# Kernel optimization log

Measured on AMD Instinct MI355X. Metric: run time of the kernel, lower is better.

## Reference

```python
import jax, jax.numpy as jnp
import numpy as np

B, T, N, D, NH = 4, 256, 8, 128, 4
SCALES = (1, 2, 3, 5)
LAGS = (1, 2, 3)
MLP_H = 32
NL_SCALE = 0.1
CMIN, CMAX = -2.5, 2.0
L_ENC = 2  # num_attn_layers


def _ln(x, g, b, eps=1e-5):
    m = x.mean(-1, keepdims=True)
    v = ((x - m) ** 2).mean(-1, keepdims=True)
    return (x - m) * jax.lax.rsqrt(v + eps) * g + b


def _gelu(x):
    return jax.nn.gelu(x, approximate=False)


def _mha(q, k, v, Wq, bq, Wk, bk, Wv, bv, Wo, bo, nh):
    Bq, Lq, Dm = q.shape
    Lk = k.shape[1]
    hd = Dm // nh
    qh = (q @ Wq.T + bq).reshape(Bq, Lq, nh, hd).transpose(0, 2, 1, 3)
    kh = (k @ Wk.T + bk).reshape(Bq, Lk, nh, hd).transpose(0, 2, 1, 3)
    vh = (v @ Wv.T + bv).reshape(Bq, Lk, nh, hd).transpose(0, 2, 1, 3)
    s = jnp.einsum('bhqd,bhkd->bhqk', qh, kh) / jnp.sqrt(jnp.float32(hd))
    p = jax.nn.softmax(s, axis=-1)
    o = jnp.einsum('bhqk,bhkd->bhqd', p, vh).transpose(0, 2, 1, 3).reshape(Bq, Lq, Dm)
    return o @ Wo.T + bo


def setup_inputs() -> dict:
    key = jax.random.key(0)
    ks = jax.random.split(key, 24)
    def w(k, shape, s=0.02):
        return s * jax.random.normal(k, shape, jnp.float32)
    inp = {}
    inp['visible_states'] = jax.random.uniform(ks[0], (B, T, N), jnp.float32) + 0.05
    inp['state_emb'] = jax.random.normal(ks[1], (B, T, N, D), jnp.float32)
    # LearnedBaseline params
    inp['r5'] = 0.1 * jnp.ones((N,), jnp.float32)
    A = 0.02 * jax.random.normal(ks[2], (N, N), jnp.float32)
    inp['A55'] = A.at[jnp.arange(N), jnp.arange(N)].set(-0.2)
    inp['bl_bias'] = jnp.zeros((N,), jnp.float32)
    inp['nl_W1'] = w(ks[3], (MLP_H, N), 0.1); inp['nl_b1'] = jnp.zeros((MLP_H,), jnp.float32)
    inp['nl_W2'] = w(ks[4], (N, MLP_H), 0.1); inp['nl_b2'] = jnp.zeros((N,), jnp.float32)
    # ResidualEncoder input MLP
    IN_DIM = len(SCALES) * (1 + len(LAGS))  # 16
    inp['mlp_W1'] = w(ks[5], (D, IN_DIM), 0.1); inp['mlp_b1'] = jnp.zeros((D,), jnp.float32)
    inp['mlp_W2'] = w(ks[6], (D, D)); inp['mlp_b2'] = jnp.zeros((D,), jnp.float32)
    inp['mlp_ln_g'] = jnp.ones((D,), jnp.float32); inp['mlp_ln_b'] = jnp.zeros((D,), jnp.float32)
    # ResidualEncoder transformer layers (stacked over L_ENC layers)
    inp['enc_qkv_W'] = w(ks[7], (L_ENC, 3 * D, D)); inp['enc_qkv_b'] = jnp.zeros((L_ENC, 3 * D), jnp.float32)
    inp['enc_out_W'] = w(ks[8], (L_ENC, D, D)); inp['enc_out_b'] = jnp.zeros((L_ENC, D), jnp.float32)
    inp['enc_ln1_g'] = jnp.ones((L_ENC, D), jnp.float32); inp['enc_ln1_b'] = jnp.zeros((L_ENC, D), jnp.float32)
    inp['enc_ff_W1'] = w(ks[9], (L_ENC, 2 * D, D)); inp['enc_ff_b1'] = jnp.zeros((L_ENC, 2 * D), jnp.float32)
    inp['enc_ff_W2'] = w(ks[10], (L_ENC, D, 2 * D)); inp['enc_ff_b2'] = jnp.zeros((L_ENC, D), jnp.float32)
    inp['enc_ln2_g'] = jnp.ones((L_ENC, D), jnp.float32); inp['enc_ln2_b'] = jnp.zeros((L_ENC, D), jnp.float32)
    # CrossAttentionFusion
    inp['ca_Wq'] = w(ks[11], (D, D)); inp['ca_bq'] = jnp.zeros((D,), jnp.float32)
    inp['ca_Wk'] = w(ks[12], (D, D)); inp['ca_bk'] = jnp.zeros((D,), jnp.float32)
    inp['ca_Wv'] = w(ks[13], (D, D)); inp['ca_bv'] = jnp.zeros((D,), jnp.float32)
    inp['ca_Wo'] = w(ks[14], (D, D)); inp['ca_bo'] = jnp.zeros((D,), jnp.float32)
    inp['ca_ln1_g'] = jnp.ones((D,), jnp.float32); inp['ca_ln1_b'] = jnp.zeros((D,), jnp.float32)
    inp['ca_ff_W1'] = w(ks[15], (4 * D, 2 * D)); inp['ca_ff_b1'] = jnp.zeros((4 * D,), jnp.float32)
    inp['ca_ff_W2'] = w(ks[16], (D, 4 * D)); inp['ca_ff_b2'] = jnp.zeros((D,), jnp.float32)
    inp['ca_ln2_g'] = jnp.ones((D,), jnp.float32); inp['ca_ln2_b'] = jnp.zeros((D,), jnp.float32)
    return inp


def _forward(visible_states, state_emb, r5, A55, bl_bias, nl_W1, nl_b1, nl_W2, nl_b2,
             mlp_W1, mlp_b1, mlp_W2, mlp_b2, mlp_ln_g, mlp_ln_b,
             enc_qkv_W, enc_qkv_b, enc_out_W, enc_out_b, enc_ln1_g, enc_ln1_b,
             enc_ff_W1, enc_ff_b1, enc_ff_W2, enc_ff_b2, enc_ln2_g, enc_ln2_b,
             ca_Wq, ca_bq, ca_Wk, ca_bk, ca_Wv, ca_bv, ca_Wo, ca_bo,
             ca_ln1_g, ca_ln1_b, ca_ff_W1, ca_ff_b1, ca_ff_W2, ca_ff_b2,
             ca_ln2_g, ca_ln2_b):
    # ---- LearnedBaseline on x_t = visible_states[:, :-1] ----
    safe = jnp.clip(visible_states, 1e-6, None)
    logx = jnp.log(safe)
    x_t = visible_states[:, :-1]  # (B,T-1,N)
    lin = r5 + jnp.einsum('btn,mn->btm', x_t, A55)
    nl = _gelu(x_t @ nl_W1.T + nl_b1) @ nl_W2.T + nl_b2
    b1 = lin + NL_SCALE * nl + bl_bias  # (B,T-1,N)
    # ---- MultiScaleResidual ----
    res_list = []
    for k in SCALES:
        actual = jnp.clip(logx[:, k:] - logx[:, :-k], CMIN * k, CMAX * k)  # (B,T-k,N)
        bk = b1[:, 0:T - k]
        for i in range(1, k):
            bk = bk + b1[:, i:i + T - k]
        res = actual - bk
        res_list.append(jnp.pad(res, ((0, 0), (0, k), (0, 0))))
    residuals = jnp.stack(res_list, axis=-1)  # (B,T,N,S)
    # ---- ResidualEncoder: takens delays ----
    feats = [residuals] + [jnp.pad(residuals, ((0, 0), (lag, 0), (0, 0), (0, 0)))[:, :T]
                           for lag in LAGS]
    x = jnp.concatenate(feats, axis=-1)  # (B,T,N,16)
    x = _gelu(x @ mlp_W1.T + mlp_b1)
    x = _gelu(x @ mlp_W2.T + mlp_b2)
    x = _ln(x, mlp_ln_g, mlp_ln_b)
    # sinusoidal PE over time
    pos = jnp.arange(T, dtype=jnp.float32)[:, None]
    div = jnp.exp(jnp.arange(0, D, 2, dtype=jnp.float32) * (-jnp.log(10000.0) / D))
    pe = jnp.stack([jnp.sin(pos * div), jnp.cos(pos * div)], axis=-1).reshape(T, D)
    x = x + pe[None, :, None, :]
    # temporal self-attention over (B*N, T, D)
    xt = x.transpose(0, 2, 1, 3).reshape(B * N, T, D)
    for i in range(L_ENC):
        Wq, Wk, Wv = jnp.split(enc_qkv_W[i], 3, axis=0)
        bq, bk_, bv = jnp.split(enc_qkv_b[i], 3)
        a = _mha(xt, xt, xt, Wq, bq, Wk, bk_, Wv, bv, enc_out_W[i], enc_out_b[i], NH)
        xt = _ln(xt + a, enc_ln1_g[i], enc_ln1_b[i])
        ff = _gelu(xt @ enc_ff_W1[i].T + enc_ff_b1[i]) @ enc_ff_W2[i].T + enc_ff_b2[i]
        xt = _ln(xt + ff, enc_ln2_g[i], enc_ln2_b[i])
    residual_emb = xt.reshape(B, N, T, D).transpose(0, 2, 1, 3)  # (B,T,N,D)
    # ---- CrossAttentionFusion ----
    s = state_emb.reshape(B, T * N, D)
    r = residual_emb.reshape(B, T * N, D)
    a = _mha(s, r, r, ca_Wq, ca_bq, ca_Wk, ca_bk, ca_Wv, ca_bv, ca_Wo, ca_bo, NH)
    s = _ln(s + a, ca_ln1_g, ca_ln1_b)
    fused = _gelu(jnp.concatenate([s, r], axis=-1) @ ca_ff_W1.T + ca_ff_b1) @ ca_ff_W2.T + ca_ff_b2
    out = _ln(s + fused, ca_ln2_g, ca_ln2_b)
    return out.reshape(B, T, N, D)


def reference(visible_states, state_emb, r5, A55, bl_bias, nl_W1, nl_b1, nl_W2, nl_b2,
              mlp_W1, mlp_b1, mlp_W2, mlp_b2, mlp_ln_g, mlp_ln_b,
              enc_qkv_W, enc_qkv_b, enc_out_W, enc_out_b, enc_ln1_g, enc_ln1_b,
              enc_ff_W1, enc_ff_b1, enc_ff_W2, enc_ff_b2, enc_ln2_g, enc_ln2_b,
              ca_Wq, ca_bq, ca_Wk, ca_bk, ca_Wv, ca_bv, ca_Wo, ca_bo,
              ca_ln1_g, ca_ln1_b, ca_ff_W1, ca_ff_b1, ca_ff_W2, ca_ff_b2,
              ca_ln2_g, ca_ln2_b):
    return _forward(visible_states, state_emb, r5, A55, bl_bias, nl_W1, nl_b1, nl_W2, nl_b2,
                    mlp_W1, mlp_b1, mlp_W2, mlp_b2, mlp_ln_g, mlp_ln_b,
                    enc_qkv_W, enc_qkv_b, enc_out_W, enc_out_b, enc_ln1_g, enc_ln1_b,
                    enc_ff_W1, enc_ff_b1, enc_ff_W2, enc_ff_b2, enc_ln2_g, enc_ln2_b,
                    ca_Wq, ca_bq, ca_Wk, ca_bk, ca_Wv, ca_bv, ca_Wo, ca_bo,
                    ca_ln1_g, ca_ln1_b, ca_ff_W1, ca_ff_b1, ca_ff_W2, ca_ff_b2,
                    ca_ln2_g, ca_ln2_b)
```

## Files before the change

### kernel.cpp

```cpp
#include <hip/hip_runtime.h>
#include <math.h>

#define B_ 4
#define T_ 256
#define N_ 8
#define D_ 128
#define NH_ 4
#define HD_ 32
#define LENC_ 2
#define MLPH_ 32
#define NL_SCALE_ 0.1f

typedef __bf16 bf16;
typedef __attribute__((ext_vector_type(2))) __bf16 bf16x2;
typedef __attribute__((ext_vector_type(4))) __bf16 bf16x4;
typedef __attribute__((ext_vector_type(8))) __bf16 bf16x8;
typedef __attribute__((ext_vector_type(4))) float f32x4;

__device__ __forceinline__ f32x4 pv_mfma16(bf16x4 a, bf16x4 b, f32x4 c) {
#if __has_builtin(__builtin_amdgcn_mfma_f32_16x16x16_bf16)
    return __builtin_amdgcn_mfma_f32_16x16x16_bf16(a, b, c, 0, 0, 0);
#else
    typedef __attribute__((ext_vector_type(4))) short s4;
    union U { bf16x4 h; s4 s; };
    U ua, ub; ua.h = a; ub.h = b;
    return __builtin_amdgcn_mfma_f32_16x16x16bf16_1k(ua.s, ub.s, c, 0, 0, 0);
#endif
}

__device__ __forceinline__ float gelu_f(float x) {
    return 0.5f * x * (1.0f + erff(x * 0.7071067811865476f));
}

__global__ void k_prep(const float* __restrict__ eqkvW, const float* __restrict__ eoutW,
                       const float* __restrict__ eff1, const float* __restrict__ eff2,
                       const float* __restrict__ wq, const float* __restrict__ wk,
                       const float* __restrict__ wv, const float* __restrict__ wo,
                       const float* __restrict__ cff1, const float* __restrict__ cff2,
                       const float* __restrict__ mlpW2, const float* __restrict__ semb,
                       const float* __restrict__ bk, const float* __restrict__ bv,
                       bf16* __restrict__ Wpk, bf16* __restrict__ sembh,
                       float* __restrict__ bpk) {
    int i = blockIdx.x * 256 + threadIdx.x;
    if (i < 540672) {
        const float* src; int off;
        if      (i < 98304)  { src = eqkvW; off = 0; }
        else if (i < 131072) { src = eoutW; off = 98304; }
        else if (i < 196608) { src = eff1;  off = 131072; }
        else if (i < 262144) { src = eff2;  off = 196608; }
        else if (i < 278528) { src = wq;    off = 262144; }
        else if (i < 294912) { src = wk;    off = 278528; }
        else if (i < 311296) { src = wv;    off = 294912; }
        else if (i < 327680) { src = wo;    off = 311296; }
        else if (i < 458752) { src = cff1;  off = 327680; }
        else if (i < 524288) { src = cff2;  off = 458752; }
        else                 { src = mlpW2; off = 524288; }
        Wpk[i] = (bf16)src[i - off];
    } else if (i < 540672 + 1048576) {
        int j = i - 540672;
        sembh[j] = (bf16)semb[j];
    } else if (i < 540672 + 1048576 + 256) {
        int t = i - 540672 - 1048576;
        bpk[t] = (t < 128) ? bk[t] : bv[t - 128];
    }
}

__global__ void k_b1(const float* __restrict__ vs, const float* __restrict__ r5,
                     const float* __restrict__ A55, const float* __restrict__ bl_bias,
                     const float* __restrict__ nlW1, const float* __restrict__ nlb1,
                     const float* __restrict__ nlW2, const float* __restrict__ nlb2,
                     float* __restrict__ b1w) {
    int idx = blockIdx.x * blockDim.x + threadIdx.x;
    if (idx >= B_ * (T_ - 1)) return;
    int b = idx / (T_ - 1), t = idx % (T_ - 1);
    float x[N_];
    for (int n = 0; n < N_; n++) x[n] = vs[(b * T_ + t) * N_ + n];
    float h[MLPH_];
    for (int j = 0; j < MLPH_; j++) {
        float a = nlb1[j];
        for (int n = 0; n < N_; n++) a += x[n] * nlW1[j * N_ + n];
        h[j] = gelu_f(a);
    }
    for (int m = 0; m < N_; m++) {
        float lin = r5[m];
        for (int n = 0; n < N_; n++) lin += x[n] * A55[m * N_ + n];
        float nl = nlb2[m];
        for (int j = 0; j < MLPH_; j++) nl += h[j] * nlW2[m * MLPH_ + j];
        b1w[idx * N_ + m] = lin + NL_SCALE_ * nl + bl_bias[m];
    }
}

__global__ void k_mlp1(const float* __restrict__ vs, const float* __restrict__ b1w,
                       const float* __restrict__ W1, const float* __restrict__ b1,
                       bf16* __restrict__ H1h) {
    int tok = blockIdx.x;
    int d = threadIdx.x;
    int b = tok >> 11, t = (tok >> 3) & 255, n = tok & 7;
    __shared__ float f[16];
    if (d < 16) {
        const int SC[4] = {1, 2, 3, 5};
        int lag = d >> 2, si = d & 3, k = SC[si];
        int tp = t - lag;
        float r = 0.0f;
        if (tp >= 0 && tp < T_ - k) {
            float lx0 = logf(fmaxf(vs[(b * T_ + tp) * N_ + n], 1e-6f));
            float lx1 = logf(fmaxf(vs[(b * T_ + tp + k) * N_ + n], 1e-6f));
            float a = lx1 - lx0;
            a = fminf(fmaxf(a, -2.5f * (float)k), 2.0f * (float)k);
            float bk = 0.0f;
            for (int i = 0; i < k; i++) bk += b1w[(b * (T_ - 1) + tp + i) * N_ + n];
            r = a - bk;
        }
        f[d] = r;
    }
    __syncthreads();
    float a = b1[d];
    const float* w = W1 + d * 16;
#pragma unroll
    for (int c = 0; c < 16; c++) a += f[c] * w[c];
    H1h[(size_t)tok * 128 + d] = (bf16)gelu_f(a);
}

__device__ __forceinline__ void gemm4_body(
    int bid, const bf16* __restrict__ A, const bf16* __restrict__ W,
    const float* __restrict__ bias, float* __restrict__ Cf,
    bf16* __restrict__ Ch, bf16* __restrict__ dq, bf16* __restrict__ dk,
    bf16* __restrict__ dvv, int N, int K, int act, int mode) {
    int lane = threadIdx.x & 63;
    int wv = threadIdx.x >> 6;
    int c = lane & 15, g = lane >> 4;
    int nN = N >> 6;
    int tn = bid % nN, tm = bid / nN;
    int row0 = tm * 64 + wv * 16;
    int cb = tn * 64;

    const bf16x8* Ap  = (const bf16x8*)(A + (size_t)(row0 + c) * K) + g;
    const bf16x8* Wp0 = (const bf16x8*)(W + (size_t)(cb + c) * K) + g;
    const bf16x8* Wp1 = (const bf16x8*)(W + (size_t)(cb + 16 + c) * K) + g;
    const bf16x8* Wp2 = (const bf16x8*)(W + (size_t)(cb + 32 + c) * K) + g;
    const bf16x8* Wp3 = (const bf16x8*)(W + (size_t)(cb + 48 + c) * K) + g;
    f32x4 a0 = {0, 0, 0, 0}, a1 = {0, 0, 0, 0};
    f32x4 a2 = {0, 0, 0, 0}, a3 = {0, 0, 0, 0};
    int nk = K >> 5;
    for (int k = 0; k < nk; k++) {
        bf16x8 av = Ap[k * 4];
        a0 = __builtin_amdgcn_mfma_f32_16x16x32_bf16(av, Wp0[k * 4], a0, 0, 0, 0);
        a1 = __builtin_amdgcn_mfma_f32_16x16x32_bf16(av, Wp1[k * 4], a1, 0, 0, 0);
        a2 = __builtin_amdgcn_mfma_f32_16x16x32_bf16(av, Wp2[k * 4], a2, 0, 0, 0);
        a3 = __builtin_amdgcn_mfma_f32_16x16x32_bf16(av, Wp3[k * 4], a3, 0, 0, 0);
    }
    int rowb = row0 + g * 4;
#pragma unroll
    for (int ct = 0; ct < 4; ct++) {
        f32x4 acc = (ct == 0) ? a0 : (ct == 1) ? a1 : (ct == 2) ? a2 : a3;
        int col = cb + ct * 16 + c;
        float bvv = bias[col];
#pragma unroll
        for (int i = 0; i < 4; i++) {
            float v = acc[i] + bvv;
            if (act) v = gelu_f(v);
            int row = rowb + i;
            if (mode == 0) {
                if (Cf) Cf[(size_t)row * N + col] = v;
                if (Ch) Ch[(size_t)row * N + col] = (bf16)v;
            } else if (mode == 1) {
                int s = row >> 8, t = row & 255;
                int h = (col >> 5) & 3, d = col & 31;
                int sh = s * 4 + h;
                if (col < 128)      dq[((size_t)sh * 256 + t) * 32 + d] = (bf16)v;
                else if (col < 256) dk[((size_t)sh * 256 + t) * 32 + d] = (bf16)v;
                else                dvv[((size_t)sh * 32 + d) * 256 + t] = (bf16)v;
            } else if (mode == 2) {
                int b = row >> 11, ll = row & 2047;
                int h = col >> 5, d = col & 31;
                dq[((size_t)(b * 4 + h) * 2048 + ll) * 32 + d] = (bf16)v;
            } else {
                int b = row >> 11, n = (row >> 8) & 7, t = row & 255;
                int ll = t * 8 + n;
                int h = (col >> 5) & 3, d = col & 31;
                if (col < 128) dk[((size_t)(b * 4 + h) * 2048 + ll) * 32 + d] = (bf16)v;
                else           dvv[((size_t)(b * 4 + h) * 32 + d) * 2048 + ll] = (bf16)v;
            }
        }
    }
}

__global__ __launch_bounds__(256) void k_gemm4(
    const bf16* __restrict__ A, const bf16* __restrict__ W,
    const float* __restrict__ bias, bf16* __restrict__ dq,
    bf16* __restrict__ dk, bf16* __restrict__ dvv, int N, int K, int mode) {
    gemm4_body(blockIdx.x, A, W, bias, nullptr, nullptr, dq, dk, dvv,
               N, K, 0, mode);
}

__global__ __launch_bounds__(256) void k_qkvc(
    const bf16* __restrict__ sembh, const bf16* __restrict__ Wq,
    const float* __restrict__ bq, const bf16* __restrict__ X0h,
    const bf16* __restrict__ Wkv, const float* __restrict__ bkv,
    bf16* __restrict__ Qh, bf16* __restrict__ Kh, bf16* __restrict__ Vth) {
    if (blockIdx.x < 256)
        gemm4_body(blockIdx.x, sembh, Wq, bq, nullptr, nullptr,
                   Qh, nullptr, nullptr, 128, 128, 0, 2);
    else
        gemm4_body(blockIdx.x - 256, X0h, Wkv, bkv, nullptr, nullptr,
                   nullptr, Kh, Vth, 256, 128, 0, 3);
}

__global__ __launch_bounds__(256) void k_gemm_ln(
    const bf16* __restrict__ A, const bf16* __restrict__ W,
    const float* __restrict__ bias, int K,
    const float* __restrict__ resf,
    const float* __restrict__ g, const float* __restrict__ be,
    float* __restrict__ outf, bf16* __restrict__ outh, int hs, int flags) {
    __shared__ float S[32][132];
    int tid = threadIdx.x;
    int w = tid >> 6, lane = tid & 63;
    int c = lane & 15, gq = lane >> 4;
    int r0 = blockIdx.x * 32 + (w >> 1) * 16;
    int cb = (w & 1) * 64;

    const bf16x8* Ap  = (const bf16x8*)(A + (size_t)(r0 + c) * K) + gq;
    const bf16x8* Wp0 = (const bf16x8*)(W + (size_t)(cb + c) * K) + gq;
    const bf16x8* Wp1 = (const bf16x8*)(W + (size_t)(cb + 16 + c) * K) + gq;
    const bf16x8* Wp2 = (const bf16x8*)(W + (size_t)(cb + 32 + c) * K) + gq;
    const bf16x8* Wp3 = (const bf16x8*)(W + (size_t)(cb + 48 + c) * K) + gq;
    f32x4 a0 = {0, 0, 0, 0}, a1 = {0, 0, 0, 0};
    f32x4 a2 = {0, 0, 0, 0}, a3 = {0, 0, 0, 0};
    int nk = K >> 5;
    for (int k = 0; k < nk; k++) {
        bf16x8 av = Ap[k * 4];
        a0 = __builtin_amdgcn_mfma_f32_16x16x32_bf16(av, Wp0[k * 4], a0, 0, 0, 0);
        a1 = __builtin_amdgcn_mfma_f32_16x16x32_bf16(av, Wp1[k * 4], a1, 0, 0, 0);
        a2 = __builtin_amdgcn_mfma_f32_16x16x32_bf16(av, Wp2[k * 4], a2, 0, 0, 0);
        a3 = __builtin_amdgcn_mfma_f32_16x16x32_bf16(av, Wp3[k * 4], a3, 0, 0, 0);
    }
    int lrow = (w >> 1) * 16 + gq * 4;
    float b0 = bias[cb + c], b1v = bias[cb + 16 + c];
    float b2v = bias[cb + 32 + c], b3v = bias[cb + 48 + c];
#pragma unroll
    for (int r = 0; r < 4; r++) {
        float v0 = a0[r] + b0, v1 = a1[r] + b1v;
        float v2 = a2[r] + b2v, v3 = a3[r] + b3v;
        if (flags & 1) {
            v0 = gelu_f(v0); v1 = gelu_f(v1); v2 = gelu_f(v2); v3 = gelu_f(v3);
        }
        S[lrow + r][cb + c] = v0;       S[lrow + r][cb + 16 + c] = v1;
        S[lrow + r][cb + 32 + c] = v2;  S[lrow + r][cb + 48 + c] = v3;
    }
    __syncthreads();

    int row = tid >> 3, cg = tid & 7;
    int grow = blockIdx.x * 32 + row;
    int b = grow >> 11, t = (grow >> 3) & 255, n = grow & 7;
    int orow = (flags & 4) ? ((b * 8 + n) * 256 + t) : grow;
    float v[16];
#pragma unroll
    for (int j = 0; j < 16; j++) v[j] = S[row][cg * 16 + j];
    if (resf) {
        const float4* rp = (const float4*)(resf + (size_t)grow * 128 + cg * 16);
#pragma unroll
        for (int j4 = 0; j4 < 4; j4++) {
            float4 rv = rp[j4];
            v[4 * j4 + 0] += rv.x; v[4 * j4 + 1] += rv.y;
            v[4 * j4 + 2] += rv.z; v[4 * j4 + 3] += rv.w;
        }
    }
    float s = 0.0f;
#pragma unroll
    for (int j = 0; j < 16; j++) s += v[j];
    s += __shfl_xor(s, 1); s += __shfl_xor(s, 2); s += __shfl_xor(s, 4);
    float mean = s * (1.0f / 128.0f);
    float vs = 0.0f;
#pragma unroll
    for (int j = 0; j < 16; j++) { float d = v[j] - mean; vs += d * d; }
    vs += __shfl_xor(vs, 1); vs += __shfl_xor(vs, 2); vs += __shfl_xor(vs, 4);
    float rstd = rsqrtf(vs * (1.0f / 128.0f) + 1e-5f);
    float y[16];
#pragma unroll
    for (int j = 0; j < 16; j++) {
        int col = cg * 16 + j;
        y[j] = (v[j] - mean) * rstd * g[col] + be[col];
    }
    if (flags & 2) {
#pragma unroll
        for (int jj = 0; jj < 8; jj++) {
            int j2 = cg * 8 + jj;
            float freq = expf((float)(2 * j2) * (-9.210340371976184f / 128.0f));
            float ang = (float)t * freq;
            y[2 * jj] += sinf(ang);
            y[2 * jj + 1] += cosf(ang);
        }
    }
    if (outf) {
        float4* op = (float4*)(outf + (size_t)orow * 128 + cg * 16);
#pragma unroll
        for (int j4 = 0; j4 < 4; j4++) {
            float4 o; o.x = y[4 * j4]; o.y = y[4 * j4 + 1];
            o.z = y[4 * j4 + 2]; o.w = y[4 * j4 + 3];
            op[j4] = o;
        }
    }
    if (outh) {
        bf16x8* op = (bf16x8*)(outh + (size_t)orow * hs + cg * 16);
#pragma unroll
        for (int j8 = 0; j8 < 2; j8++) {
            bf16x8 o;
#pragma unroll
            for (int e = 0; e < 8; e++) o[e] = (bf16)y[8 * j8 + e];
            op[j8] = o;
        }
    }
}

__global__ __launch_bounds__(256) void k_enc_tail(
    const bf16* __restrict__ ATTh, const bf16* __restrict__ Wo,
    const float* __restrict__ bo, const float* __restrict__ X0res,
    const float* __restrict__ g1, const float* __restrict__ be1,
    const bf16* __restrict__ W1, const float* __restrict__ bf1,
    const bf16* __restrict__ W2, const float* __restrict__ bf2,
    const float* __restrict__ g2, const float* __restrict__ be2,
    float* __restrict__ X0out, bf16* __restrict__ X0hout) {
    __shared__ float S[32][132];
    __shared__ float X1f[32][132];
    __shared__ bf16 X1h[32][136];
    __shared__ bf16 H[32][264];
    int tid = threadIdx.x;
    int w = tid >> 6, lane = tid & 63;
    int c = lane & 15, gq = lane >> 4;
    int r0l = (w >> 1) * 16;
    int cb = (w & 1) * 64;
    int blk = blockIdx.x;
    const f32x4 zero = {0, 0, 0, 0};

    {
        const bf16x8* Ap  = (const bf16x8*)(ATTh + (size_t)(blk * 32 + r0l + c) * 128) + gq;
        const bf16x8* Wp0 = (const bf16x8*)(Wo + (size_t)(cb + c) * 128) + gq;
        const bf16x8* Wp1 = (const bf16x8*)(Wo + (size_t)(cb + 16 + c) * 128) + gq;
        const bf16x8* Wp2 = (const bf16x8*)(Wo + (size_t)(cb + 32 + c) * 128) + gq;
        const bf16x8* Wp3 = (const bf16x8*)(Wo + (size_t)(cb + 48 + c) * 128) + gq;
        f32x4 a0 = zero, a1 = zero, a2 = zero, a3 = zero;
#pragma unroll
        for (int k = 0; k < 4; k++) {
            bf16x8 av = Ap[k * 4];
            a0 = __builtin_amdgcn_mfma_f32_16x16x32_bf16(av, Wp0[k * 4], a0, 0, 0, 0);
            a1 = __builtin_amdgcn_mfma_f32_16x16x32_bf16(av, Wp1[k * 4], a1, 0, 0, 0);
            a2 = __builtin_amdgcn_mfma_f32_16x16x32_bf16(av, Wp2[k * 4], a2, 0, 0, 0);
            a3 = __builtin_amdgcn_mfma_f32_16x16x32_bf16(av, Wp3[k * 4], a3, 0, 0, 0);
        }
        int lrow = r0l + gq * 4;
        float b0 = bo[cb + c], b1v = bo[cb + 16 + c];
        float b2v = bo[cb + 32 + c], b3v = bo[cb + 48 + c];
#pragma unroll
        for (int r = 0; r < 4; r++) {
            S[lrow + r][cb + c] = a0[r] + b0;
            S[lrow + r][cb + 16 + c] = a1[r] + b1v;
            S[lrow + r][cb + 32 + c] = a2[r] + b2v;
            S[lrow + r][cb + 48 + c] = a3[r] + b3v;
        }
    }
    __syncthreads();
    {
        int row = tid >> 3, cg = tid & 7;
        float v[16];
        const float4* rp = (const float4*)(X0res + (size_t)(blk * 32 + row) * 128 + cg * 16);
#pragma unroll
        for (int j4 = 0; j4 < 4; j4++) {
            float4 rv = rp[j4];
            v[4 * j4 + 0] = S[row][cg * 16 + 4 * j4 + 0] + rv.x;
            v[4 * j4 + 1] = S[row][cg * 16 + 4 * j4 + 1] + rv.y;
            v[4 * j4 + 2] = S[row][cg * 16 + 4 * j4 + 2] + rv.z;
            v[4 * j4 + 3] = S[row][cg * 16 + 4 * j4 + 3] + rv.w;
        }
        float s = 0.0f;
#pragma unroll
        for (int j = 0; j < 16; j++) s += v[j];
        s += __shfl_xor(s, 1); s += __shfl_xor(s, 2); s += __shfl_xor(s, 4);
        float mean = s * (1.0f / 128.0f);
        float vs = 0.0f;
#pragma unroll
        for (int j = 0; j < 16; j++) { float d = v[j] - mean; vs += d * d; }
        vs += __shfl_xor(vs, 1); vs += __shfl_xor(vs, 2); vs += __shfl_xor(vs, 4);
        float rstd = rsqrtf(vs * (1.0f / 128.0f) + 1e-5f);
#pragma unroll
        for (int j = 0; j < 16; j++) {
            int col = cg * 16 + j;
            float y = (v[j] - mean) * rstd * g1[col] + be1[col];
            X1f[row][col] = y;
            X1h[row][col] = (bf16)y;
        }
    }
    __syncthreads();
    {
        bf16x8 af[4];
#pragma unroll
// ... 346 lines not shown
        s += __shfl_xor(s, 16);
        s += __shfl_xor(s, 32);
        if (g == 0) L_lds[wv][qt * 16 + c] = s;
        *(f32x4*)&O_lds[wv][qt * 16 + c][g * 4] = oT[qt][0];
        *(f32x4*)&O_lds[wv][qt * 16 + c][16 + g * 4] = oT[qt][1];
    }
    __syncthreads();

    int tid = threadIdx.x;
    int ql = tid >> 2, dq = (tid & 3) * 8;
    float ltot = L_lds[0][ql] + L_lds[1][ql] + L_lds[2][ql] + L_lds[3][ql];
    float inv = 1.0f / ltot;
    float acc[8];
#pragma unroll
    for (int j = 0; j < 8; j++) acc[j] = 0.0f;
#pragma unroll
    for (int w = 0; w < 4; w++) {
        const float* p = &O_lds[w][ql][dq];
#pragma unroll
        for (int j = 0; j < 8; j++) acc[j] += p[j];
    }
    int h = sh & 3, sb = sh >> 2;
    bf16x8 o;
#pragma unroll
    for (int j = 0; j < 8; j++) o[j] = (bf16)(acc[j] * inv);
    *(bf16x8*)(ATTh + ((size_t)sb * Lq + q0 + ql) * 128 + h * 32 + dq) = o;
}

extern "C" void kernel_launch(void* const* d_in, const int* in_sizes, int n_in,
                              void* d_out, int out_size, void* d_ws, size_t ws_size,
                              hipStream_t stream) {
    const float* vs       = (const float*)d_in[0];
    const float* semb     = (const float*)d_in[1];
    const float* r5       = (const float*)d_in[2];
    const float* A55      = (const float*)d_in[3];
    const float* bl_bias  = (const float*)d_in[4];
    const float* nl_W1    = (const float*)d_in[5];
    const float* nl_b1    = (const float*)d_in[6];
    const float* nl_W2    = (const float*)d_in[7];
    const float* nl_b2    = (const float*)d_in[8];
    const float* mlp_W1   = (const float*)d_in[9];
    const float* mlp_b1   = (const float*)d_in[10];
    const float* mlp_W2   = (const float*)d_in[11];
    const float* mlp_b2   = (const float*)d_in[12];
    const float* mlp_ln_g = (const float*)d_in[13];
    const float* mlp_ln_b = (const float*)d_in[14];
    const float* enc_qkv_W = (const float*)d_in[15];
    const float* enc_qkv_b = (const float*)d_in[16];
    const float* enc_out_W = (const float*)d_in[17];
    const float* enc_out_b = (const float*)d_in[18];
    const float* enc_ln1_g = (const float*)d_in[19];
    const float* enc_ln1_b = (const float*)d_in[20];
    const float* enc_ff_W1 = (const float*)d_in[21];
    const float* enc_ff_b1 = (const float*)d_in[22];
    const float* enc_ff_W2 = (const float*)d_in[23];
    const float* enc_ff_b2 = (const float*)d_in[24];
    const float* enc_ln2_g = (const float*)d_in[25];
    const float* enc_ln2_b = (const float*)d_in[26];
    const float* ca_Wq = (const float*)d_in[27];
    const float* ca_bq = (const float*)d_in[28];
    const float* ca_Wk = (const float*)d_in[29];
    const float* ca_bk = (const float*)d_in[30];
    const float* ca_Wv = (const float*)d_in[31];
    const float* ca_bv = (const float*)d_in[32];
    const float* ca_Wo = (const float*)d_in[33];
    const float* ca_bo = (const float*)d_in[34];
    const float* ca_ln1_g = (const float*)d_in[35];
    const float* ca_ln1_b = (const float*)d_in[36];
    const float* ca_ff_W1 = (const float*)d_in[37];
    const float* ca_ff_b1 = (const float*)d_in[38];
    const float* ca_ff_W2 = (const float*)d_in[39];
    const float* ca_ff_b2 = (const float*)d_in[40];
    const float* ca_ln2_g = (const float*)d_in[41];
    const float* ca_ln2_b = (const float*)d_in[42];
    float* out = (float*)d_out;

    char* base = (char*)d_ws;
    float* b1w   = (float*)(base + 0);
    float* X0    = (float*)(base + 163840);
    char*  QKVr  = base + 8552448;
    bf16*  Wpk   = (bf16*) (base + 25329664);
    float* bpk   = (float*)(base + 26411008);
    bf16*  X0h   = (bf16*) (base + 26412032);
    bf16*  X1h   = (bf16*) (base + 28509184);
    bf16*  sembh = (bf16*) (base + 30606336);
    bf16*  ATTh  = (bf16*) (base + 32703488);
    bf16*  Qh    = (bf16*)QKVr;
    bf16*  Kh    = (bf16*)(QKVr + 2097152);
    bf16*  Vth   = (bf16*)(QKVr + 4194304);

    const int NTOK = B_ * T_ * N_;

    k_prep<<<dim3(6209), dim3(256), 0, stream>>>(
        enc_qkv_W, enc_out_W, enc_ff_W1, enc_ff_W2, ca_Wq, ca_Wk, ca_Wv, ca_Wo,
        ca_ff_W1, ca_ff_W2, mlp_W2, semb, ca_bk, ca_bv, Wpk, sembh, bpk);

    k_b1<<<dim3((B_ * (T_ - 1) + 63) / 64), dim3(64), 0, stream>>>(
        vs, r5, A55, bl_bias, nl_W1, nl_b1, nl_W2, nl_b2, b1w);
    k_mlp1<<<dim3(NTOK), dim3(128), 0, stream>>>(vs, b1w, mlp_W1, mlp_b1, X1h);
    k_gemm_ln<<<dim3(256), dim3(256), 0, stream>>>(
        X1h, Wpk + 524288, mlp_b2, 128, nullptr, mlp_ln_g, mlp_ln_b,
        X0, X0h, 128, 1 | 2 | 4);

    for (int i = 0; i < LENC_; i++) {
        k_gemm4<<<dim3(768), dim3(256), 0, stream>>>(
            X0h, Wpk + i * 49152, enc_qkv_b + i * 384, Qh, Kh, Vth, 384, 128, 1);
        k_mattn<<<dim3(512), dim3(256), 0, stream>>>(
            Qh, Kh, Vth, ATTh, 256, 256, 128);
        k_enc_tail<<<dim3(256), dim3(256), 0, stream>>>(
            ATTh, Wpk + 98304 + i * 16384, enc_out_b + i * 128, X0,
            enc_ln1_g + i * 128, enc_ln1_b + i * 128,
            Wpk + 131072 + i * 32768, enc_ff_b1 + i * 256,
            Wpk + 196608 + i * 32768, enc_ff_b2 + i * 128,
            enc_ln2_g + i * 128, enc_ln2_b + i * 128, X0, X0h);
    }

    k_qkvc<<<dim3(768), dim3(256), 0, stream>>>(
        sembh, Wpk + 262144, ca_bq, X0h, Wpk + 278528, bpk, Qh, Kh, Vth);
    k_mattn<<<dim3(512), dim3(256), 0, stream>>>(
        Qh, Kh, Vth, ATTh, 2048, 2048, 16);
    k_cross_tail<<<dim3(256), dim3(256), 0, stream>>>(
        ATTh, Wpk + 311296, ca_bo, semb, ca_ln1_g, ca_ln1_b, X0h,
        Wpk + 327680, ca_ff_b1, Wpk + 458752, ca_ff_b2,
        ca_ln2_g, ca_ln2_b, out);
}
```

Measured before the change: 338.2 us.

## Fuse prep with baseline, MLP with LayerNorm, and encoder QKV with attention

Merges the weight-packing kernel and the baseline-residual kernel into one launch. Fuses the input-MLP first layer into the second GEMM+LayerNorm kernel so the intermediate stays in shared memory. Replaces the encoder's separate QKV GEMM and attention kernels with one kernel per sequence and head that projects Q/K/V into LDS and runs attention there. This removes several launches and the global round-trips for H1 and Q/K/V. The cost is only 128 blocks for encoder attention, which may leave many CUs idle, plus softmax without max subtraction (relying on small scores).

Result: no change. 337.1 us (-0.3%).

```diff
diff --git a/kernel.cpp b/kernel.cpp
--- a/kernel.cpp
+++ b/kernel.cpp
@@ -32,45 +32,46 @@
     return 0.5f * x * (1.0f + erff(x * 0.7071067811865476f));
 }
 
-__global__ void k_prep(const float* __restrict__ eqkvW, const float* __restrict__ eoutW,
-                       const float* __restrict__ eff1, const float* __restrict__ eff2,
-                       const float* __restrict__ wq, const float* __restrict__ wk,
-                       const float* __restrict__ wv, const float* __restrict__ wo,
-                       const float* __restrict__ cff1, const float* __restrict__ cff2,
-                       const float* __restrict__ mlpW2, const float* __restrict__ semb,
-                       const float* __restrict__ bk, const float* __restrict__ bv,
-                       bf16* __restrict__ Wpk, bf16* __restrict__ sembh,
-                       float* __restrict__ bpk) {
-    int i = blockIdx.x * 256 + threadIdx.x;
-    if (i < 540672) {
-        const float* src; int off;
-        if      (i < 98304)  { src = eqkvW; off = 0; }
-        else if (i < 131072) { src = eoutW; off = 98304; }
-        else if (i < 196608) { src = eff1;  off = 131072; }
-        else if (i < 262144) { src = eff2;  off = 196608; }
-        else if (i < 278528) { src = wq;    off = 262144; }
-        else if (i < 294912) { src = wk;    off = 278528; }
-        else if (i < 311296) { src = wv;    off = 294912; }
-        else if (i < 327680) { src = wo;    off = 311296; }
-        else if (i < 458752) { src = cff1;  off = 327680; }
-        else if (i < 524288) { src = cff2;  off = 458752; }
-        else                 { src = mlpW2; off = 524288; }
-        Wpk[i] = (bf16)src[i - off];
-    } else if (i < 540672 + 1048576) {
-        int j = i - 540672;
-        sembh[j] = (bf16)semb[j];
-    } else if (i < 540672 + 1048576 + 256) {
-        int t = i - 540672 - 1048576;
-        bpk[t] = (t < 128) ? bk[t] : bv[t - 128];
-    }
-}
-
-__global__ void k_b1(const float* __restrict__ vs, const float* __restrict__ r5,
-                     const float* __restrict__ A55, const float* __restrict__ bl_bias,
-                     const float* __restrict__ nlW1, const float* __restrict__ nlb1,
-                     const float* __restrict__ nlW2, const float* __restrict__ nlb2,
-                     float* __restrict__ b1w) {
-    int idx = blockIdx.x * blockDim.x + threadIdx.x;
+__global__ void k_prep_b1(const float* __restrict__ eqkvW, const float* __restrict__ eoutW,
+                          const float* __restrict__ eff1, const float* __restrict__ eff2,
+                          const float* __restrict__ wq, const float* __restrict__ wk,
+                          const float* __restrict__ wv, const float* __restrict__ wo,
+                          const float* __restrict__ cff1, const float* __restrict__ cff2,
+                          const float* __restrict__ mlpW2, const float* __restrict__ semb,
+                          const float* __restrict__ bk, const float* __restrict__ bv,
+                          bf16* __restrict__ Wpk, bf16* __restrict__ sembh,
+                          float* __restrict__ bpk,
+                          const float* __restrict__ vs, const float* __restrict__ r5,
+                          const float* __restrict__ A55, const float* __restrict__ bl_bias,
+                          const float* __restrict__ nlW1, const float* __restrict__ nlb1,
+                          const float* __restrict__ nlW2, const float* __restrict__ nlb2,
+                          float* __restrict__ b1w) {
+    if (blockIdx.x < 6209) {
+        int i = blockIdx.x * 256 + threadIdx.x;
+        if (i < 540672) {
+            const float* src; int off;
+            if      (i < 98304)  { src = eqkvW; off = 0; }
+            else if (i < 131072) { src = eoutW; off = 98304; }
+            else if (i < 196608) { src = eff1;  off = 131072; }
+            else if (i < 262144) { src = eff2;  off = 196608; }
+            else if (i < 278528) { src = wq;    off = 262144; }
+            else if (i < 294912) { src = wk;    off = 278528; }
+            else if (i < 311296) { src = wv;    off = 294912; }
+            else if (i < 327680) { src = wo;    off = 311296; }
+            else if (i < 458752) { src = cff1;  off = 327680; }
+            else if (i < 524288) { src = cff2;  off = 458752; }
+            else                 { src = mlpW2; off = 524288; }
+            Wpk[i] = (bf16)src[i - off];
+        } else if (i < 540672 + 1048576) {
+            int j = i - 540672;
+            sembh[j] = (bf16)semb[j];
+        } else if (i < 540672 + 1048576 + 256) {
+            int t = i - 540672 - 1048576;
+            bpk[t] = (t < 128) ? bk[t] : bv[t - 128];
+        }
+        return;
+    }
+    int idx = (blockIdx.x - 6209) * 256 + threadIdx.x;
     if (idx >= B_ * (T_ - 1)) return;
     int b = idx / (T_ - 1), t = idx % (T_ - 1);
     float x[N_];
@@ -90,16 +91,24 @@
     }
 }
 
-__global__ void k_mlp1(const float* __restrict__ vs, const float* __restrict__ b1w,
-                       const float* __restrict__ W1, const float* __restrict__ b1,
-                       bf16* __restrict__ H1h) {
-    int tok = blockIdx.x;
-    int d = threadIdx.x;
-    int b = tok >> 11, t = (tok >> 3) & 255, n = tok & 7;
-    __shared__ float f[16];
-    if (d < 16) {
+__global__ __launch_bounds__(256) void k_mlp_ln(
+    const float* __restrict__ vs, const float* __restrict__ b1w,
+    const float* __restrict__ W1, const float* __restrict__ b1,
+    const bf16* __restrict__ W2, const float* __restrict__ bias,
+    const float* __restrict__ g, const float* __restrict__ be,
+    float* __restrict__ outf, bf16* __restrict__ outh) {
+    __shared__ float F[32][16];
+    __shared__ bf16 H1[32][136];
+    __shared__ float S[32][132];
+    int tid = threadIdx.x;
+    int blk = blockIdx.x;
+#pragma unroll
+    for (int e = tid; e < 512; e += 256) {
+        int row = e >> 4, feat = e & 15;
+        int grow = blk * 32 + row;
+        int b = grow >> 11, t = (grow >> 3) & 255, n = grow & 7;
         const int SC[4] = {1, 2, 3, 5};
-        int lag = d >> 2, si = d & 3, k = SC[si];
+        int lag = feat >> 2, si = feat & 3, k = SC[si];
         int tp = t - lag;
         float r = 0.0f;
         if (tp >= 0 && tp < T_ - k) {
@@ -111,21 +120,213 @@
             for (int i = 0; i < k; i++) bk += b1w[(b * (T_ - 1) + tp + i) * N_ + n];
             r = a - bk;
         }
-        f[d] = r;
-    }
-    __syncthreads();
-    float a = b1[d];
-    const float* w = W1 + d * 16;
-#pragma unroll
-    for (int c = 0; c < 16; c++) a += f[c] * w[c];
-    H1h[(size_t)tok * 128 + d] = (bf16)gelu_f(a);
+        F[row][feat] = r;
+    }
+    __syncthreads();
+    {
+        int row = tid >> 3, cg = tid & 7;
+        float f[16];
+#pragma unroll
+        for (int c = 0; c < 16; c++) f[c] = F[row][c];
+#pragma unroll
+        for (int j = 0; j < 16; j++) {
+            int d = cg * 16 + j;
+            float a = b1[d];
+            const float* w = W1 + d * 16;
+#pragma unroll
+            for (int c = 0; c < 16; c++) a += f[c] * w[c];
+            H1[row][d] = (bf16)gelu_f(a);
+        }
+    }
+    __syncthreads();
+    int w = tid >> 6, lane = tid & 63;
+    int c = lane & 15, gq = lane >> 4;
+    int r0l = (w >> 1) * 16;
+    int cb = (w & 1) * 64;
+    const f32x4 zero = {0, 0, 0, 0};
+    {
+        const bf16x8* Wp0 = (const bf16x8*)(W2 + (size_t)(cb + c) * 128) + gq;
+        const bf16x8* Wp1 = (const bf16x8*)(W2 + (size_t)(cb + 16 + c) * 128) + gq;
+        const bf16x8* Wp2 = (const bf16x8*)(W2 + (size_t)(cb + 32 + c) * 128) + gq;
+        const bf16x8* Wp3 = (const bf16x8*)(W2 + (size_t)(cb + 48 + c) * 128) + gq;
+        f32x4 a0 = zero, a1 = zero, a2 = zero, a3 = zero;
+#pragma unroll
+        for (int k = 0; k < 4; k++) {
+            bf16x8 av = *(const bf16x8*)&H1[r0l + c][k * 32 + gq * 8];
+            a0 = __builtin_amdgcn_mfma_f32_16x16x32_bf16(av, Wp0[k * 4], a0, 0, 0, 0);
+            a1 = __builtin_amdgcn_mfma_f32_16x16x32_bf16(av, Wp1[k * 4], a1, 0, 0, 0);
+            a2 = __builtin_amdgcn_mfma_f32_16x16x32_bf16(av, Wp2[k * 4], a2, 0, 0, 0);
+            a3 = __builtin_amdgcn_mfma_f32_16x16x32_bf16(av, Wp3[k * 4], a3, 0, 0, 0);
+        }
+        int lrow = r0l + gq * 4;
+#pragma unroll
+        for (int r = 0; r < 4; r++) {
+            S[lrow + r][cb + c]      = gelu_f(a0[r] + bias[cb + c]);
+            S[lrow + r][cb + 16 + c] = gelu_f(a1[r] + bias[cb + 16 + c]);
+            S[lrow + r][cb + 32 + c] = gelu_f(a2[r] + bias[cb + 32 + c]);
+            S[lrow + r][cb + 48 + c] = gelu_f(a3[r] + bias[cb + 48 + c]);
+        }
+    }
+    __syncthreads();
+    {
+        int row = tid >> 3, cg = tid & 7;
+        int grow = blk * 32 + row;
+        int b = grow >> 11, t = (grow >> 3) & 255, n = grow & 7;
+        int orow = (b * 8 + n) * 256 + t;
+        float v[16];
+#pragma unroll
+        for (int j = 0; j < 16; j++) v[j] = S[row][cg * 16 + j];
+        float s = 0.0f;
+#pragma unroll
+        for (int j = 0; j < 16; j++) s += v[j];
+        s += __shfl_xor(s, 1); s += __shfl_xor(s, 2); s += __shfl_xor(s, 4);
+        float mean = s * (1.0f / 128.0f);
+        float vs2 = 0.0f;
+#pragma unroll
+        for (int j = 0; j < 16; j++) { float d = v[j] - mean; vs2 += d * d; }
+        vs2 += __shfl_xor(vs2, 1); vs2 += __shfl_xor(vs2, 2); vs2 += __shfl_xor(vs2, 4);
+        float rstd = rsqrtf(vs2 * (1.0f / 128.0f) + 1e-5f);
+        float y[16];
+#pragma unroll
+        for (int j = 0; j < 16; j++) {
+            int col = cg * 16 + j;
+            y[j] = (v[j] - mean) * rstd * g[col] + be[col];
+        }
+#pragma unroll
+        for (int jj = 0; jj < 8; jj++) {
+            int j2 = cg * 8 + jj;
+            float freq = expf((float)(2 * j2) * (-9.210340371976184f / 128.0f));
+            float ang = (float)t * freq;
+            y[2 * jj] += sinf(ang);
+            y[2 * jj + 1] += cosf(ang);
+        }
+        float4* of = (float4*)(outf + (size_t)orow * 128 + cg * 16);
+        bf16x8* oh = (bf16x8*)(outh + (size_t)orow * 128 + cg * 16);
+#pragma unroll
+        for (int j4 = 0; j4 < 4; j4++) {
+            float4 o; o.x = y[4 * j4]; o.y = y[4 * j4 + 1];
+            o.z = y[4 * j4 + 2]; o.w = y[4 * j4 + 3];
+            of[j4] = o;
+        }
+#pragma unroll
+        for (int j8 = 0; j8 < 2; j8++) {
+            bf16x8 o;
+#pragma unroll
+            for (int e = 0; e < 8; e++) o[e] = (bf16)y[8 * j8 + e];
+            oh[j8] = o;
+        }
+    }
+}
+
+__global__ __launch_bounds__(256) void k_enc_attn(
+    const bf16* __restrict__ X0h, const bf16* __restrict__ Wqkv,
+    const float* __restrict__ bqkv, bf16* __restrict__ ATTh) {
+    int sh = blockIdx.x;
+    int s = sh >> 2, h = sh & 3;
+    __shared__ bf16 Ql[256][40];
+    __shared__ bf16 Kl[256][40];
+    __shared__ bf16 Vt[32][264];
+    int tid = threadIdx.x;
+    int wv = tid >> 6, lane = tid & 63;
+    int c = lane & 15, g = lane >> 4;
+    const f32x4 zero = {0, 0, 0, 0};
+
+    {
+        const bf16* Wq0 = Wqkv + (size_t)(h * 32 + c) * 128;
+        const bf16* Wq1 = Wqkv + (size_t)(h * 32 + 16 + c) * 128;
+        const bf16* Wk0 = Wqkv + (size_t)(128 + h * 32 + c) * 128;
+        const bf16* Wk1 = Wqkv + (size_t)(128 + h * 32 + 16 + c) * 128;
+        const bf16* Wv0 = Wqkv + (size_t)(256 + h * 32 + c) * 128;
+        const bf16* Wv1 = Wqkv + (size_t)(256 + h * 32 + 16 + c) * 128;
+        float bq0 = bqkv[h * 32 + c], bq1 = bqkv[h * 32 + 16 + c];
+        float bk0 = bqkv[128 + h * 32 + c], bk1 = bqkv[128 + h * 32 + 16 + c];
+        float bv0 = bqkv[256 + h * 32 + c], bv1 = bqkv[256 + h * 32 + 16 + c];
+#pragma unroll
+        for (int rb = 0; rb < 4; rb++) {
+            int row0 = wv * 64 + rb * 16;
+            const bf16x8* Ap = (const bf16x8*)(X0h + (size_t)(s * 256 + row0 + c) * 128) + g;
+            f32x4 aq0 = zero, aq1 = zero, ak0 = zero, ak1 = zero, av0 = zero, av1 = zero;
+#pragma unroll
+            for (int k = 0; k < 4; k++) {
+                bf16x8 av = Ap[k * 4];
+                aq0 = __builtin_amdgcn_mfma_f32_16x16x32_bf16(av, *((const bf16x8*)Wq0 + k * 4 + g), aq0, 0, 0, 0);
+                aq1 = __builtin_amdgcn_mfma_f32_16x16x32_bf16(av, *((const bf16x8*)Wq1 + k * 4 + g), aq1, 0, 0, 0);
+                ak0 = __builtin_amdgcn_mfma_f32_16x16x32_bf16(av, *((const bf16x8*)Wk0 + k * 4 + g), ak0, 0, 0, 0);
+                ak1 = __builtin_amdgcn_mfma_f32_16x16x32_bf16(av, *((const bf16x8*)Wk1 + k * 4 + g), ak1, 0, 0, 0);
+                av0 = __builtin_amdgcn_mfma_f32_16x16x32_bf16(av, *((const bf16x8*)Wv0 + k * 4 + g), av0, 0, 0, 0);
+                av1 = __builtin_amdgcn_mfma_f32_16x16x32_bf16(av, *((const bf16x8*)Wv1 + k * 4 + g), av1, 0, 0, 0);
+            }
+            int lr = row0 + g * 4;
+#pragma unroll
+            for (int i = 0; i < 4; i++) {
+                Ql[lr + i][c] = (bf16)(aq0[i] + bq0);
+                Ql[lr + i][16 + c] = (bf16)(aq1[i] + bq1);
+                Kl[lr + i][c] = (bf16)(ak0[i] + bk0);
+                Kl[lr + i][16 + c] = (bf16)(ak1[i] + bk1);
+                Vt[c][lr + i] = (bf16)(av0[i] + bv0);
+                Vt[16 + c][lr + i] = (bf16)(av1[i] + bv1);
+            }
+        }
+    }
+    __syncthreads();
+
+    const float scale = 0.17677669529663687f;
+    int q0 = wv * 64;
+    bf16x8 bq[4];
+#pragma unroll
+    for (int qt = 0; qt < 4; qt++)
+        bq[qt] = *(const bf16x8*)&Ql[q0 + qt * 16 + c][g * 8];
+    f32x4 oT[4][2];
+#pragma unroll
+    for (int qt = 0; qt < 4; qt++) { oT[qt][0] = zero; oT[qt][1] = zero; }
+    float lsum[4] = {0, 0, 0, 0};
+#pragma unroll
+    for (int t = 0; t < 8; t++) {
+        int k0 = t * 32;
+        bf16x8 ka = *(const bf16x8*)&Kl[k0 + c][g * 8];
+        bf16x8 kb = *(const bf16x8*)&Kl[k0 + 16 + c][g * 8];
+        bf16x4 va0 = *(const bf16x4*)&Vt[c][k0 + g * 4];
+        bf16x4 va1 = *(const bf16x4*)&Vt[c][k0 + 16 + g * 4];
+        bf16x4 vb0 = *(const bf16x4*)&Vt[16 + c][k0 + g * 4];
+        bf16x4 vb1 = *(const bf16x4*)&Vt[16 + c][k0 + 16 + g * 4];
+#pragma unroll
+        for (int qt = 0; qt < 4; qt++) {
+            f32x4 s0 = __builtin_amdgcn_mfma_f32_16x16x32_bf16(ka, bq[qt], zero, 0, 0, 0);
+            f32x4 s1 = __builtin_amdgcn_mfma_f32_16x16x32_bf16(kb, bq[qt], zero, 0, 0, 0);
+            bf16x4 p0, p1;
+#pragma unroll
+            for (int r = 0; r < 4; r++) {
+                float e0 = __expf(s0[r] * scale);
+                float e1 = __expf(s1[r] * scale);
+                lsum[qt] += e0 + e1;
+                p0[r] = (bf16)e0;
+                p1[r] = (bf16)e1;
+            }
+            oT[qt][0] = pv_mfma16(va0, p0, oT[qt][0]);
+            oT[qt][0] = pv_mfma16(va1, p1, oT[qt][0]);
+            oT[qt][1] = pv_mfma16(vb0, p0, oT[qt][1]);
+            oT[qt][1] = pv_mfma16(vb1, p1, oT[qt][1]);
+        }
+    }
+#pragma unroll
+    for (int qt = 0; qt < 4; qt++) {
+        float sm = lsum[qt];
+        sm += __shfl_xor(sm, 16);
+        sm += __shfl_xor(sm, 32);
+        float inv = 1.0f / sm;
+        size_t rbase = ((size_t)s * 256 + q0 + qt * 16 + c) * 128 + h * 32;
+#pragma unroll
+        for (int r = 0; r < 4; r++) {
+            ATTh[rbase + g * 4 + r] = (bf16)(oT[qt][0][r] * inv);
+            ATTh[rbase + 16 + g * 4 + r] = (bf16)(oT[qt][1][r] * inv);
+        }
+    }
 }
 
 __device__ __forceinline__ void gemm4_body(
     int bid, const bf16* __restrict__ A, const bf16* __restrict__ W,
-    const float* __restrict__ bias, float* __restrict__ Cf,
-    bf16* __restrict__ Ch, bf16* __restrict__ dq, bf16* __restrict__ dk,
-    bf16* __restrict__ dvv, int N, int K, int act, int mode) {
+    const float* __restrict__ bias, bf16* __restrict__ dq,
+    bf16* __restrict__ dk, bf16* __restrict__ dvv, int N, int K, int mode) {
     int lane = threadIdx.x & 63;
     int wv = threadIdx.x >> 6;
     int c = lane & 15, g = lane >> 4;
@@ -158,39 +359,20 @@
 #pragma unroll
         for (int i = 0; i < 4; i++) {
             float v = acc[i] + bvv;
-            if (act) v = gelu_f(v);
             int row = rowb + i;
-            if (mode == 0) {
-                if (Cf) Cf[(size_t)row * N + col] = v;
-                if (Ch) Ch[(size_t)row * N + col] = (bf16)v;
-            } else if (mode == 1) {
-                int s = row >> 8, t = row & 255;
-                int h = (col >> 5) & 3, d = col & 31;
-                int sh = s * 4 + h;
-                if (col < 128)      dq[((size_t)sh * 256 + t) * 32 + d] = (bf16)v;
-                else if (col < 256) dk[((size_t)sh * 256 + t) * 32 + d] = (bf16)v;
-                else                dvv[((size_t)sh * 32 + d) * 256 + t] = (bf16)v;
-            } else if (mode == 2) {
+            if (mode == 2) {
                 int b = row >> 11, ll = row & 2047;
-                int h = col >> 5, d = col & 31;
-                dq[((size_t)(b * 4 + h) * 2048 + ll) * 32 + d] = (bf16)v;
+                int hh = col >> 5, d = col & 31;
+                dq[((size_t)(b * 4 + hh) * 2048 + ll) * 32 + d] = (bf16)v;
             } else {
                 int b = row >> 11, n = (row >> 8) & 7, t = row & 255;
                 int ll = t * 8 + n;
-                int h = (col >> 5) & 3, d = col & 31;
-                if (col < 128) dk[((size_t)(b * 4 + h) * 2048 + ll) * 32 + d] = (bf16)v;
-                else           dvv[((size_t)(b * 4 + h) * 32 + d) * 2048 + ll] = (bf16)v;
+                int hh = (col >> 5) & 3, d = col & 31;
+                if (col < 128) dk[((size_t)(b * 4 + hh) * 2048 + ll) * 32 + d] = (bf16)v;
+                else           dvv[((size_t)(b * 4 + hh) * 32 + d) * 2048 + ll] = (bf16)v;
             }
         }
     }
-}
-
-__global__ __launch_bounds__(256) void k_gemm4(
-    const bf16* __restrict__ A, const bf16* __restrict__ W,
-    const float* __restrict__ bias, bf16* __restrict__ dq,
-    bf16* __restrict__ dk, bf16* __restrict__ dvv, int N, int K, int mode) {
-    gemm4_body(blockIdx.x, A, W, bias, nullptr, nullptr, dq, dk, dvv,
-               N, K, 0, mode);
 }
 
 __global__ __launch_bounds__(256) void k_qkvc(
@@ -199,117 +381,9 @@
     const bf16* __restrict__ Wkv, const float* __restrict__ bkv,
     bf16* __restrict__ Qh, bf16* __restrict__ Kh, bf16* __restrict__ Vth) {
     if (blockIdx.x < 256)
-        gemm4_body(blockIdx.x, sembh, Wq, bq, nullptr, nullptr,
-                   Qh, nullptr, nullptr, 128, 128, 0, 2);
+        gemm4_body(blockIdx.x, sembh, Wq, bq, Qh, nullptr, nullptr, 128, 128, 2);
     else
-        gemm4_body(blockIdx.x - 256, X0h, Wkv, bkv, nullptr, nullptr,
-                   nullptr, Kh, Vth, 256, 128, 0, 3);
-}
-
-__global__ __launch_bounds__(256) void k_gemm_ln(
-    const bf16* __restrict__ A, const bf16* __restrict__ W,
-    const float* __restrict__ bias, int K,
-    const float* __restrict__ resf,
-    const float* __restrict__ g, const float* __restrict__ be,
-    float* __restrict__ outf, bf16* __restrict__ outh, int hs, int flags) {
-    __shared__ float S[32][132];
-    int tid = threadIdx.x;
-    int w = tid >> 6, lane = tid & 63;
-    int c = lane & 15, gq = lane >> 4;
-    int r0 = blockIdx.x * 32 + (w >> 1) * 16;
-    int cb = (w & 1) * 64;
-
-    const bf16x8* Ap  = (const bf16x8*)(A + (size_t)(r0 + c) * K) + gq;
-    const bf16x8* Wp0 = (const bf16x8*)(W + (size_t)(cb + c) * K) + gq;
-    const bf16x8* Wp1 = (const bf16x8*)(W + (size_t)(cb + 16 + c) * K) + gq;
-    const bf16x8* Wp2 = (const bf16x8*)(W + (size_t)(cb + 32 + c) * K) + gq;
-    const bf16x8* Wp3 = (const bf16x8*)(W + (size_t)(cb + 48 + c) * K) + gq;
-    f32x4 a0 = {0, 0, 0, 0}, a1 = {0, 0, 0, 0};
-    f32x4 a2 = {0, 0, 0, 0}, a3 = {0, 0, 0, 0};
-    int nk = K >> 5;
-    for (int k = 0; k < nk; k++) {
-        bf16x8 av = Ap[k * 4];
-        a0 = __builtin_amdgcn_mfma_f32_16x16x32_bf16(av, Wp0[k * 4], a0, 0, 0, 0);
-        a1 = __builtin_amdgcn_mfma_f32_16x16x32_bf16(av, Wp1[k * 4], a1, 0, 0, 0);
-        a2 = __builtin_amdgcn_mfma_f32_16x16x32_bf16(av, Wp2[k * 4], a2, 0, 0, 0);
-        a3 = __builtin_amdgcn_mfma_f32_16x16x32_bf16(av, Wp3[k * 4], a3, 0, 0, 0);
-    }
-    int lrow = (w >> 1) * 16 + gq * 4;
-    float b0 = bias[cb + c], b1v = bias[cb + 16 + c];
-    float b2v = bias[cb + 32 + c], b3v = bias[cb + 48 + c];
-#pragma unroll
-    for (int r = 0; r < 4; r++) {
-        float v0 = a0[r] + b0, v1 = a1[r] + b1v;
-        float v2 = a2[r] + b2v, v3 = a3[r] + b3v;
-        if (flags & 1) {
-            v0 = gelu_f(v0); v1 = gelu_f(v1); v2 = gelu_f(v2); v3 = gelu_f(v3);
-        }
-        S[lrow + r][cb + c] = v0;       S[lrow + r][cb + 16 + c] = v1;
-        S[lrow + r][cb + 32 + c] = v2;  S[lrow + r][cb + 48 + c] = v3;
-    }
-    __syncthreads();
-
-    int row = tid >> 3, cg = tid & 7;
-    int grow = blockIdx.x * 32 + row;
-    int b = grow >> 11, t = (grow >> 3) & 255, n = grow & 7;
-    int orow = (flags & 4) ? ((b * 8 + n) * 256 + t) : grow;
-    float v[16];
-#pragma unroll
-    for (int j = 0; j < 16; j++) v[j] = S[row][cg * 16 + j];
-    if (resf) {
-        const float4* rp = (const float4*)(resf + (size_t)grow * 128 + cg * 16);
-#pragma unroll
-        for (int j4 = 0; j4 < 4; j4++) {
-            float4 rv = rp[j4];
-            v[4 * j4 + 0] += rv.x; v[4 * j4 + 1] += rv.y;
-            v[4 * j4 + 2] += rv.z; v[4 * j4 + 3] += rv.w;
-        }
-    }
-    float s = 0.0f;
-#pragma unroll
-    for (int j = 0; j < 16; j++) s += v[j];
-    s += __shfl_xor(s, 1); s += __shfl_xor(s, 2); s += __shfl_xor(s, 4);
-    float mean = s * (1.0f / 128.0f);
-    float vs = 0.0f;
-#pragma unroll
-    for (int j = 0; j < 16; j++) { float d = v[j] - mean; vs += d * d; }
-    vs += __shfl_xor(vs, 1); vs += __shfl_xor(vs, 2); vs += __shfl_xor(vs, 4);
-    float rstd = rsqrtf(vs * (1.0f / 128.0f) + 1e-5f);
-    float y[16];
-#pragma unroll
-    for (int j = 0; j < 16; j++) {
-        int col = cg * 16 + j;
-        y[j] = (v[j] - mean) * rstd * g[col] + be[col];
-    }
-    if (flags & 2) {
-#pragma unroll
-        for (int jj = 0; jj < 8; jj++) {
-            int j2 = cg * 8 + jj;
-            float freq = expf((float)(2 * j2) * (-9.210340371976184f / 128.0f));
-            float ang = (float)t * freq;
-            y[2 * jj] += sinf(ang);
-            y[2 * jj + 1] += cosf(ang);
-        }
-    }
-    if (outf) {
-        float4* op = (float4*)(outf + (size_t)orow * 128 + cg * 16);
-#pragma unroll
-        for (int j4 = 0; j4 < 4; j4++) {
-            float4 o; o.x = y[4 * j4]; o.y = y[4 * j4 + 1];
-            o.z = y[4 * j4 + 2]; o.w = y[4 * j4 + 3];
-            op[j4] = o;
-        }
-    }
-    if (outh) {
-        bf16x8* op = (bf16x8*)(outh + (size_t)orow * hs + cg * 16);
-#pragma unroll
-        for (int j8 = 0; j8 < 2; j8++) {
-            bf16x8 o;
-#pragma unroll
-            for (int e = 0; e < 8; e++) o[e] = (bf16)y[8 * j8 + e];
-            op[j8] = o;
-        }
-    }
+        gemm4_body(blockIdx.x - 256, X0h, Wkv, bkv, nullptr, Kh, Vth, 256, 128, 3);
 }
 
 __global__ __launch_bounds__(256) void k_enc_tail(
@@ -822,31 +896,24 @@
     bf16*  Wpk   = (bf16*) (base + 25329664);
     float* bpk   = (float*)(base + 26411008);
     bf16*  X0h   = (bf16*) (base + 26412032);
-    bf16*  X1h   = (bf16*) (base + 28509184);
     bf16*  sembh = (bf16*) (base + 30606336);
     bf16*  ATTh  = (bf16*) (base + 32703488);
     bf16*  Qh    = (bf16*)QKVr;
     bf16*  Kh    = (bf16*)(QKVr + 2097152);
     bf16*  Vth   = (bf16*)(QKVr + 4194304);
 
-    const int NTOK = B_ * T_ * N_;
-
-    k_prep<<<dim3(6209), dim3(256), 0, stream>>>(
+    k_prep_b1<<<dim3(6213), dim3(256), 0, stream>>>(
         enc_qkv_W, enc_out_W, enc_ff_W1, enc_ff_W2, ca_Wq, ca_Wk, ca_Wv, ca_Wo,
-        ca_ff_W1, ca_ff_W2, mlp_W2, semb, ca_bk, ca_bv, Wpk, sembh, bpk);
-
-    k_b1<<<dim3((B_ * (T_ - 1) + 63) / 64), dim3(64), 0, stream>>>(
+        ca_ff_W1, ca_ff_W2, mlp_W2, semb, ca_bk, ca_bv, Wpk, sembh, bpk,
         vs, r5, A55, bl_bias, nl_W1, nl_b1, nl_W2, nl_b2, b1w);
-    k_mlp1<<<dim3(NTOK), dim3(128), 0, stream>>>(vs, b1w, mlp_W1, mlp_b1, X1h);
-    k_gemm_ln<<<dim3(256), dim3(256), 0, stream>>>(
-        X1h, Wpk + 524288, mlp_b2, 128, nullptr, mlp_ln_g, mlp_ln_b,
-        X0, X0h, 128, 1 | 2 | 4);
+
+    k_mlp_ln<<<dim3(256), dim3(256), 0, stream>>>(
+        vs, b1w, mlp_W1, mlp_b1, Wpk + 524288, mlp_b2, mlp_ln_g, mlp_ln_b,
+        X0, X0h);
 
     for (int i = 0; i < LENC_; i++) {
-        k_gemm4<<<dim3(768), dim3(256), 0, stream>>>(
-            X0h, Wpk + i * 49152, enc_qkv_b + i * 384, Qh, Kh, Vth, 384, 128, 1);
-        k_mattn<<<dim3(512), dim3(256), 0, stream>>>(
-            Qh, Kh, Vth, ATTh, 256, 256, 128);
+        k_enc_attn<<<dim3(128), dim3(256), 0, stream>>>(
+            X0h, Wpk + i * 49152, enc_qkv_b + i * 384, ATTh);
         k_enc_tail<<<dim3(256), dim3(256), 0, stream>>>(
             ATTh, Wpk + 98304 + i * 16384, enc_out_b + i * 128, X0,
             enc_ln1_g + i * 128, enc_ln1_b + i * 128,
```
